# Performance work log

Measured on AMD Instinct MI355X. Metric: run time of the kernel, lower is better.

The kernel has to match this reference:

```python
import jax, jax.numpy as jnp
import numpy as np

SEQ_LEN, BATCH, TAGS = 512, 1024, 32
START_IDX, END_IDX = 30, 31
NEG = -10000.0


def setup_inputs() -> dict:
    key = jax.random.key(0)
    k1, k2 = jax.random.split(key)
    feats = jax.random.normal(k1, (SEQ_LEN, BATCH, TAGS), dtype=jnp.float32)
    mask = jnp.ones((SEQ_LEN, BATCH), dtype=jnp.float32)
    # xavier-normal-ish transition, then apply START/END constraints as in reset_parameters
    transition = jax.random.normal(k2, (TAGS, TAGS), dtype=jnp.float32) * (2.0 / (TAGS + TAGS)) ** 0.5
    transition = transition.at[START_IDX, :].set(NEG)
    transition = transition.at[:, END_IDX].set(NEG)
    return {"feats": feats, "mask": mask, "transition": transition}


def reference(feats, mask, transition):
    # feats: (T, N, M), mask: (T, N), transition: (M, M)
    batch_size, tag_size = feats.shape[1], feats.shape[2]
    alpha0 = jnp.full((batch_size, tag_size), NEG, dtype=feats.dtype)
    alpha0 = alpha0.at[:, START_IDX].set(0.0)

    def step(alpha, inp):
        feat_t, mask_t = inp  # (N, M), (N,)
        # score[n, j, i] = alpha[n, i] + transition[j, i] + feat[n, j]
        score = alpha[:, None, :] + transition[None, :, :] + feat_t[:, :, None]
        new_alpha = jax.nn.logsumexp(score, axis=-1)  # (N, M)
        m = mask_t[:, None]
        alpha = new_alpha * m + alpha * (1.0 - m)
        return alpha, None

    alpha, _ = jax.lax.scan(step, alpha0, (feats, mask))
    alpha = alpha + transition[END_IDX][None, :]
    return jax.nn.logsumexp(alpha, axis=-1)  # (N,)
```

## Files before the change

kernel.cpp:

```cpp
#include <hip/hip_runtime.h>


constexpr int SEQ = 512, BATCH = 1024, TAGS = 32;
constexpr int NC = 8, L = SEQ / NC;
constexpr int RSTRIDE = 36;

#define LOG2E 1.4426950408889634f
#define LN2   0.6931471805599453f

typedef __attribute__((ext_vector_type(8))) short short8;
typedef __attribute__((ext_vector_type(4))) float float4v;
union Frag8 { unsigned u[4]; short8 v; };

__device__ __forceinline__ unsigned pk_rn(float x, float y) {
  return __builtin_amdgcn_perm(__float_as_uint(y) + 0x8000u,
                               __float_as_uint(x) + 0x8000u, 0x07060302u);
}
__device__ __forceinline__ unsigned pk_tr(float x, float y) {
  return __builtin_amdgcn_perm(__float_as_uint(y), __float_as_uint(x), 0x07060302u);
}

__device__ __forceinline__ void mm32(const float* __restrict__ A,
                                     const float* __restrict__ Bs,
                                     int s, int q, float4v D[4]) {
  Frag8 fa0, fa1, fb0, fb1;
  const float* ar0 = A + s * RSTRIDE;
  const float* ar1 = A + (16 + s) * RSTRIDE;
  fa0.u[0] = pk_rn(ar0[4 * q + 0], ar0[4 * q + 1]);
  fa0.u[1] = pk_rn(ar0[4 * q + 2], ar0[4 * q + 3]);
  fa0.u[2] = pk_rn(ar0[16 + 4 * q + 0], ar0[16 + 4 * q + 1]);
  fa0.u[3] = pk_rn(ar0[16 + 4 * q + 2], ar0[16 + 4 * q + 3]);
  fa1.u[0] = pk_rn(ar1[4 * q + 0], ar1[4 * q + 1]);
  fa1.u[1] = pk_rn(ar1[4 * q + 2], ar1[4 * q + 3]);
  fa1.u[2] = pk_rn(ar1[16 + 4 * q + 0], ar1[16 + 4 * q + 1]);
  fa1.u[3] = pk_rn(ar1[16 + 4 * q + 2], ar1[16 + 4 * q + 3]);
  fb0.u[0] = pk_rn(Bs[(4 * q + 0) * RSTRIDE + s], Bs[(4 * q + 1) * RSTRIDE + s]);
  fb0.u[1] = pk_rn(Bs[(4 * q + 2) * RSTRIDE + s], Bs[(4 * q + 3) * RSTRIDE + s]);
  fb0.u[2] = pk_rn(Bs[(16 + 4 * q + 0) * RSTRIDE + s], Bs[(16 + 4 * q + 1) * RSTRIDE + s]);
  fb0.u[3] = pk_rn(Bs[(16 + 4 * q + 2) * RSTRIDE + s], Bs[(16 + 4 * q + 3) * RSTRIDE + s]);
  fb1.u[0] = pk_rn(Bs[(4 * q + 0) * RSTRIDE + 16 + s], Bs[(4 * q + 1) * RSTRIDE + 16 + s]);
  fb1.u[1] = pk_rn(Bs[(4 * q + 2) * RSTRIDE + 16 + s], Bs[(4 * q + 3) * RSTRIDE + 16 + s]);
  fb1.u[2] = pk_rn(Bs[(16 + 4 * q + 0) * RSTRIDE + 16 + s], Bs[(16 + 4 * q + 1) * RSTRIDE + 16 + s]);
  fb1.u[3] = pk_rn(Bs[(16 + 4 * q + 2) * RSTRIDE + 16 + s], Bs[(16 + 4 * q + 3) * RSTRIDE + 16 + s]);
  const float4v z = {0.f, 0.f, 0.f, 0.f};
  D[0] = __builtin_amdgcn_mfma_f32_16x16x32_bf16(fa0.v, fb0.v, z, 0, 0, 0);
  D[1] = __builtin_amdgcn_mfma_f32_16x16x32_bf16(fa0.v, fb1.v, z, 0, 0, 0);
  D[2] = __builtin_amdgcn_mfma_f32_16x16x32_bf16(fa1.v, fb0.v, z, 0, 0, 0);
  D[3] = __builtin_amdgcn_mfma_f32_16x16x32_bf16(fa1.v, fb1.v, z, 0, 0, 0);
}

__device__ __forceinline__ void wrD(float* __restrict__ W, int s, int q,
                                    const float4v D[4]) {
#pragma unroll
  for (int p = 0; p < 4; ++p) {
    W[(4 * q + p) * RSTRIDE + s]           = D[0][p];
    W[(4 * q + p) * RSTRIDE + 16 + s]      = D[1][p];
    W[(16 + 4 * q + p) * RSTRIDE + s]      = D[2][p];
    W[(16 + 4 * q + p) * RSTRIDE + 16 + s] = D[3][p];
  }
}

extern "C" __global__ void __launch_bounds__(512, 4) crf_fused(
    const float* __restrict__ feats, const float* __restrict__ mask,
    const float* __restrict__ trans, float* __restrict__ out) {
  __shared__ float gshare[8][66 * RSTRIDE];
  __shared__ float c2s[8];
  const int wid_u = __builtin_amdgcn_readfirstlane((int)(threadIdx.x >> 6));
  const int lane = threadIdx.x & 63;
  const int b = blockIdx.x;
  const int c = wid_u;
  const int s = lane & 15, q = lane >> 4;
  float* Wf = &gshare[wid_u][0];

  unsigned long long mb;
  {
    const float* fro = feats + ((size_t)(c * L + lane) * BATCH + b) * TAGS;
    float4v fv[8];
#pragma unroll
    for (int i = 0; i < 8; ++i) fv[i] = *(const float4v*)(fro + 4 * i);
    const float mv = mask[(size_t)(c * L + lane) * BATCH + b];
    mb = __ballot(mv != 0.0f);
#pragma unroll
    for (int i = 0; i < 8; ++i) {
      float4v ev;
      ev[0] = __builtin_amdgcn_exp2f(fv[i][0] * LOG2E);
      ev[1] = __builtin_amdgcn_exp2f(fv[i][1] * LOG2E);
      ev[2] = __builtin_amdgcn_exp2f(fv[i][2] * LOG2E);
      ev[3] = __builtin_amdgcn_exp2f(fv[i][3] * LOG2E);
      *(float4v*)(Wf + lane * RSTRIDE + 4 * i) = ev;
    }
  }

  int sig[8];
#pragma unroll
  for (int i = 0; i < 8; ++i) sig[i] = (i < 4) ? (4 * q + i) : (16 + 4 * q + (i - 4));
  Frag8 e0, e1;
#pragma unroll
  for (int p = 0; p < 4; ++p) {
    e0.u[p] = pk_rn(__builtin_amdgcn_exp2f(trans[s * TAGS + sig[2 * p]] * LOG2E),
                    __builtin_amdgcn_exp2f(trans[s * TAGS + sig[2 * p + 1]] * LOG2E));
    e1.u[p] = pk_rn(__builtin_amdgcn_exp2f(trans[(16 + s) * TAGS + sig[2 * p]] * LOG2E),
                    __builtin_amdgcn_exp2f(trans[(16 + s) * TAGS + sig[2 * p + 1]] * LOG2E));
  }
  float ef0[4], ef1[4];
#pragma unroll
  for (int p = 0; p < 4; ++p) {
    ef0[p] = __builtin_amdgcn_exp2f(trans[31 * TAGS + (4 * q + p)] * LOG2E);
    ef1[p] = __builtin_amdgcn_exp2f(trans[31 * TAGS + (16 + 4 * q + p)] * LOG2E);
  }

  float4v P00 = {0,0,0,0}, P01 = {0,0,0,0}, P10 = {0,0,0,0}, P11 = {0,0,0,0};
#pragma unroll
  for (int p = 0; p < 4; ++p) {
    float one = (4 * q + p == s) ? 1.f : 0.f;
    P00[p] = one; P11[p] = one;
  }
  Frag8 B0, B1;
  float c2 = 0.f;
  const float4v zerov = {0.f, 0.f, 0.f, 0.f};

#define PACK_B()                                                        \
  { B0.u[0] = pk_tr(P00[0], P00[1]); B0.u[1] = pk_tr(P00[2], P00[3]);   \
    B0.u[2] = pk_tr(P10[0], P10[1]); B0.u[3] = pk_tr(P10[2], P10[3]);   \
    B1.u[0] = pk_tr(P01[0], P01[1]); B1.u[1] = pk_tr(P01[2], P01[3]);   \
    B1.u[2] = pk_tr(P11[0], P11[1]); B1.u[3] = pk_tr(P11[2], P11[3]); }
  PACK_B()

#define RDF0(t) (*(const float4v*)(Wf + (t) * RSTRIDE + q * 4))
#define RDF1(t) (*(const float4v*)(Wf + (t) * RSTRIDE + 16 + q * 4))

  float4v F0a = RDF0(0), F1a = RDF1(0), F0b = RDF0(1), F1b = RDF1(1);

#pragma unroll 8
  for (int r = 0; r < L; ++r) {
    const float4v F0 = (r & 1) ? F0b : F0a;
    const float4v F1 = (r & 1) ? F1b : F1a;
    if (r & 1) { F0b = RDF0(r + 2); F1b = RDF1(r + 2); }
    else       { F0a = RDF0(r + 2); F1a = RDF1(r + 2); }

    if ((mb >> r) & 1ull) {
      float4v D00 = __builtin_amdgcn_mfma_f32_16x16x32_bf16(e0.v, B0.v, zerov, 0, 0, 0);
      float4v D01 = __builtin_amdgcn_mfma_f32_16x16x32_bf16(e0.v, B1.v, zerov, 0, 0, 0);
      float4v D10 = __builtin_amdgcn_mfma_f32_16x16x32_bf16(e1.v, B0.v, zerov, 0, 0, 0);
      float4v D11 = __builtin_amdgcn_mfma_f32_16x16x32_bf16(e1.v, B1.v, zerov, 0, 0, 0);
      P00 = D00 * F0; P01 = D01 * F0;
      P10 = D10 * F1; P11 = D11 * F1;
      PACK_B()
    }

    if ((r & 7) == 7) {
      float4v m4 = __builtin_elementwise_max(__builtin_elementwise_max(P00, P01),
                                             __builtin_elementwise_max(P10, P11));
      float mx = fmaxf(fmaxf(m4[0], m4[1]), fmaxf(m4[2], m4[3]));
      mx = fmaxf(mx, __shfl_xor(mx, 1, 64));
      mx = fmaxf(mx, __shfl_xor(mx, 2, 64));
      mx = fmaxf(mx, __shfl_xor(mx, 4, 64));
      mx = fmaxf(mx, __shfl_xor(mx, 8, 64));
      mx = fmaxf(mx, __shfl_xor(mx, 16, 64));
      mx = fmaxf(mx, __shfl_xor(mx, 32, 64));
      int ex = (int)((__float_as_uint(mx) >> 23) & 0xFFu) - 127;
      float scl = __uint_as_float((unsigned)(127 - ex) << 23);
      P00 *= scl; P01 *= scl; P10 *= scl; P11 *= scl;
      c2 += (float)ex;
      PACK_B()
    }
  }

  __builtin_amdgcn_s_waitcnt(0);
  __builtin_amdgcn_wave_barrier();
  {
    float4v Pv[4] = {P00, P01, P10, P11};
    wrD(Wf, s, q, Pv);
  }
  if (lane == 0) c2s[wid_u] = c2;
  __syncthreads();

  float4v Dm[4];
  if (wid_u < 4) {
    mm32(&gshare[2 * wid_u + 1][0], &gshare[2 * wid_u][0], s, q, Dm);
    wrD(&gshare[2 * wid_u][0], s, q, Dm);
  }
  __syncthreads();
  if (wid_u < 2) {
    mm32(&gshare[4 * wid_u + 2][0], &gshare[4 * wid_u][0], s, q, Dm);
    wrD(&gshare[4 * wid_u][0], s, q, Dm);
  }
  __syncthreads();
  if (wid_u == 0) {
    mm32(&gshare[4][0], &gshare[0][0], s, q, Dm);
    float vv = 0.f;
#pragma unroll
    for (int p = 0; p < 4; ++p) vv += ef0[p] * Dm[1][p] + ef1[p] * Dm[3][p];
    vv += __shfl_xor(vv, 16, 64);
    vv += __shfl_xor(vv, 32, 64);
    float c2t = ((c2s[0] + c2s[1]) + (c2s[2] + c2s[3])) +
                ((c2s[4] + c2s[5]) + (c2s[6] + c2s[7]));
    if (lane == 14) out[b] = LN2 * (c2t + __builtin_amdgcn_logf(vv));
  }
}

extern "C" void kernel_launch(void* const* d_in, const int* in_sizes, int n_in,
                              void* d_out, int out_size, void* d_ws, size_t ws_size,
                              hipStream_t stream) {
  const float* feats = (const float*)d_in[0];
  const float* mask  = (const float*)d_in[1];
  const float* trans = (const float*)d_in[2];
  float* out = (float*)d_out;
  hipLaunchKernelGGL(crf_fused, dim3(BATCH), dim3(512), 0, stream,
                     feats, mask, trans, out);
}
```

Before: 128.2 us.

## Store exp(feats) as packed bf16 in LDS and replace matrix tree with vector sweep

Exponentiated emissions are now packed in pairs as bf16 into a smaller, XOR-swizzled LDS buffer, which shrinks shared memory per block. That shrinkage lets launch bounds request eight blocks per CU instead of four. The final combine of the eight chunk transfer matrices no longer uses a log-depth tree of 32x32 MFMA products. It instead propagates the END-row vector backwards through each wave's matrix sequentially, with per-step renormalisation. The cost is lower emission precision (bf16 instead of fp32 in the elementwise multiply), eight serialized barrier steps, and possible register pressure from the doubled occupancy target.

```diff
diff --git a/kernel.cpp b/kernel.cpp
--- a/kernel.cpp
+++ b/kernel.cpp
@@ -3,13 +3,14 @@
 
 constexpr int SEQ = 512, BATCH = 1024, TAGS = 32;
 constexpr int NC = 8, L = SEQ / NC;
-constexpr int RSTRIDE = 36;
+constexpr int RROW = 16;
 
 #define LOG2E 1.4426950408889634f
 #define LN2   0.6931471805599453f
 
 typedef __attribute__((ext_vector_type(8))) short short8;
 typedef __attribute__((ext_vector_type(4))) float float4v;
+typedef __attribute__((ext_vector_type(4))) unsigned uint4v;
 union Frag8 { unsigned u[4]; short8 v; };
 
 __device__ __forceinline__ unsigned pk_rn(float x, float y) {
@@ -20,74 +21,43 @@
   return __builtin_amdgcn_perm(__float_as_uint(y), __float_as_uint(x), 0x07060302u);
 }
 
-__device__ __forceinline__ void mm32(const float* __restrict__ A,
-                                     const float* __restrict__ Bs,
-                                     int s, int q, float4v D[4]) {
-  Frag8 fa0, fa1, fb0, fb1;
-  const float* ar0 = A + s * RSTRIDE;
-  const float* ar1 = A + (16 + s) * RSTRIDE;
-  fa0.u[0] = pk_rn(ar0[4 * q + 0], ar0[4 * q + 1]);
-  fa0.u[1] = pk_rn(ar0[4 * q + 2], ar0[4 * q + 3]);
-  fa0.u[2] = pk_rn(ar0[16 + 4 * q + 0], ar0[16 + 4 * q + 1]);
-  fa0.u[3] = pk_rn(ar0[16 + 4 * q + 2], ar0[16 + 4 * q + 3]);
-  fa1.u[0] = pk_rn(ar1[4 * q + 0], ar1[4 * q + 1]);
-  fa1.u[1] = pk_rn(ar1[4 * q + 2], ar1[4 * q + 3]);
-  fa1.u[2] = pk_rn(ar1[16 + 4 * q + 0], ar1[16 + 4 * q + 1]);
-  fa1.u[3] = pk_rn(ar1[16 + 4 * q + 2], ar1[16 + 4 * q + 3]);
-  fb0.u[0] = pk_rn(Bs[(4 * q + 0) * RSTRIDE + s], Bs[(4 * q + 1) * RSTRIDE + s]);
-  fb0.u[1] = pk_rn(Bs[(4 * q + 2) * RSTRIDE + s], Bs[(4 * q + 3) * RSTRIDE + s]);
-  fb0.u[2] = pk_rn(Bs[(16 + 4 * q + 0) * RSTRIDE + s], Bs[(16 + 4 * q + 1) * RSTRIDE + s]);
-  fb0.u[3] = pk_rn(Bs[(16 + 4 * q + 2) * RSTRIDE + s], Bs[(16 + 4 * q + 3) * RSTRIDE + s]);
-  fb1.u[0] = pk_rn(Bs[(4 * q + 0) * RSTRIDE + 16 + s], Bs[(4 * q + 1) * RSTRIDE + 16 + s]);
-  fb1.u[1] = pk_rn(Bs[(4 * q + 2) * RSTRIDE + 16 + s], Bs[(4 * q + 3) * RSTRIDE + 16 + s]);
-  fb1.u[2] = pk_rn(Bs[(16 + 4 * q + 0) * RSTRIDE + 16 + s], Bs[(16 + 4 * q + 1) * RSTRIDE + 16 + s]);
-  fb1.u[3] = pk_rn(Bs[(16 + 4 * q + 2) * RSTRIDE + 16 + s], Bs[(16 + 4 * q + 3) * RSTRIDE + 16 + s]);
-  const float4v z = {0.f, 0.f, 0.f, 0.f};
-  D[0] = __builtin_amdgcn_mfma_f32_16x16x32_bf16(fa0.v, fb0.v, z, 0, 0, 0);
-  D[1] = __builtin_amdgcn_mfma_f32_16x16x32_bf16(fa0.v, fb1.v, z, 0, 0, 0);
-  D[2] = __builtin_amdgcn_mfma_f32_16x16x32_bf16(fa1.v, fb0.v, z, 0, 0, 0);
-  D[3] = __builtin_amdgcn_mfma_f32_16x16x32_bf16(fa1.v, fb1.v, z, 0, 0, 0);
-}
-
-__device__ __forceinline__ void wrD(float* __restrict__ W, int s, int q,
-                                    const float4v D[4]) {
-#pragma unroll
-  for (int p = 0; p < 4; ++p) {
-    W[(4 * q + p) * RSTRIDE + s]           = D[0][p];
-    W[(4 * q + p) * RSTRIDE + 16 + s]      = D[1][p];
-    W[(16 + 4 * q + p) * RSTRIDE + s]      = D[2][p];
-    W[(16 + 4 * q + p) * RSTRIDE + 16 + s] = D[3][p];
-  }
-}
-
-extern "C" __global__ void __launch_bounds__(512, 4) crf_fused(
+extern "C" __global__ void __launch_bounds__(512, 8) crf_fused(
     const float* __restrict__ feats, const float* __restrict__ mask,
     const float* __restrict__ trans, float* __restrict__ out) {
-  __shared__ float gshare[8][66 * RSTRIDE];
-  __shared__ float c2s[8];
-  const int wid_u = __builtin_amdgcn_readfirstlane((int)(threadIdx.x >> 6));
+  __shared__ unsigned gst[NC][66 * RROW];
+  __shared__ float c2s[NC];
+  __shared__ __align__(16) float ws[TAGS];
+  __shared__ float c2x;
+
+  const int wid = __builtin_amdgcn_readfirstlane((int)(threadIdx.x >> 6));
   const int lane = threadIdx.x & 63;
   const int b = blockIdx.x;
-  const int c = wid_u;
   const int s = lane & 15, q = lane >> 4;
-  float* Wf = &gshare[wid_u][0];
+  unsigned* Wp = &gst[wid][0];
 
   unsigned long long mb;
   {
-    const float* fro = feats + ((size_t)(c * L + lane) * BATCH + b) * TAGS;
+    const float* fro = feats + ((size_t)(wid * L + lane) * BATCH + b) * TAGS;
     float4v fv[8];
 #pragma unroll
     for (int i = 0; i < 8; ++i) fv[i] = *(const float4v*)(fro + 4 * i);
-    const float mv = mask[(size_t)(c * L + lane) * BATCH + b];
+    const float mv = mask[(size_t)(wid * L + lane) * BATCH + b];
     mb = __ballot(mv != 0.0f);
+    unsigned Upk[16];
 #pragma unroll
-    for (int i = 0; i < 8; ++i) {
-      float4v ev;
-      ev[0] = __builtin_amdgcn_exp2f(fv[i][0] * LOG2E);
-      ev[1] = __builtin_amdgcn_exp2f(fv[i][1] * LOG2E);
-      ev[2] = __builtin_amdgcn_exp2f(fv[i][2] * LOG2E);
-      ev[3] = __builtin_amdgcn_exp2f(fv[i][3] * LOG2E);
-      *(float4v*)(Wf + lane * RSTRIDE + 4 * i) = ev;
+    for (int j = 0; j < 16; ++j) {
+      const float lo = __builtin_amdgcn_exp2f(fv[j >> 2][j & 3] * LOG2E);
+      const float hi = __builtin_amdgcn_exp2f(fv[4 + (j >> 2)][j & 3] * LOG2E);
+      Upk[j] = pk_rn(lo, hi);
+    }
+    const int swr = ((lane >> 1) & 3) << 2;
+    unsigned* rp = Wp + lane * RROW;
+#pragma unroll
+    for (int g = 0; g < 16; g += 4) {
+      uint4v t;
+#pragma unroll
+      for (int k2 = 0; k2 < 4; ++k2) t[k2] = Upk[(g ^ swr) + k2];
+      *(uint4v*)(rp + g) = t;
     }
   }
 
@@ -102,14 +72,8 @@
     e1.u[p] = pk_rn(__builtin_amdgcn_exp2f(trans[(16 + s) * TAGS + sig[2 * p]] * LOG2E),
                     __builtin_amdgcn_exp2f(trans[(16 + s) * TAGS + sig[2 * p + 1]] * LOG2E));
   }
-  float ef0[4], ef1[4];
-#pragma unroll
-  for (int p = 0; p < 4; ++p) {
-    ef0[p] = __builtin_amdgcn_exp2f(trans[31 * TAGS + (4 * q + p)] * LOG2E);
-    ef1[p] = __builtin_amdgcn_exp2f(trans[31 * TAGS + (16 + 4 * q + p)] * LOG2E);
-  }
 
-  float4v P00 = {0,0,0,0}, P01 = {0,0,0,0}, P10 = {0,0,0,0}, P11 = {0,0,0,0};
+  float4v P00 = {0, 0, 0, 0}, P01 = {0, 0, 0, 0}, P10 = {0, 0, 0, 0}, P11 = {0, 0, 0, 0};
 #pragma unroll
   for (int p = 0; p < 4; ++p) {
     float one = (4 * q + p == s) ? 1.f : 0.f;
@@ -126,19 +90,22 @@
     B1.u[2] = pk_tr(P11[0], P11[1]); B1.u[3] = pk_tr(P11[2], P11[3]); }
   PACK_B()
 
-#define RDF0(t) (*(const float4v*)(Wf + (t) * RSTRIDE + q * 4))
-#define RDF1(t) (*(const float4v*)(Wf + (t) * RSTRIDE + 16 + q * 4))
+#define RDU(t) (*(const uint4v*)(Wp + (t) * RROW + ((4 * q) ^ ((((t) >> 1) & 3) << 2))))
 
-  float4v F0a = RDF0(0), F1a = RDF1(0), F0b = RDF0(1), F1b = RDF1(1);
+  uint4v Ua = RDU(0), Ub = RDU(1);
 
 #pragma unroll 8
   for (int r = 0; r < L; ++r) {
-    const float4v F0 = (r & 1) ? F0b : F0a;
-    const float4v F1 = (r & 1) ? F1b : F1a;
-    if (r & 1) { F0b = RDF0(r + 2); F1b = RDF1(r + 2); }
-    else       { F0a = RDF0(r + 2); F1a = RDF1(r + 2); }
+    const uint4v U = (r & 1) ? Ub : Ua;
+    if (r & 1) Ub = RDU(r + 2); else Ua = RDU(r + 2);
 
     if ((mb >> r) & 1ull) {
+      float4v F0, F1;
+#pragma unroll
+      for (int i = 0; i < 4; ++i) {
+        F0[i] = __uint_as_float(U[i] << 16);
+        F1[i] = __uint_as_float(U[i] & 0xffff0000u);
+      }
       float4v D00 = __builtin_amdgcn_mfma_f32_16x16x32_bf16(e0.v, B0.v, zerov, 0, 0, 0);
       float4v D01 = __builtin_amdgcn_mfma_f32_16x16x32_bf16(e0.v, B1.v, zerov, 0, 0, 0);
       float4v D10 = __builtin_amdgcn_mfma_f32_16x16x32_bf16(e1.v, B0.v, zerov, 0, 0, 0);
@@ -166,36 +133,49 @@
     }
   }
 
-  __builtin_amdgcn_s_waitcnt(0);
-  __builtin_amdgcn_wave_barrier();
-  {
-    float4v Pv[4] = {P00, P01, P10, P11};
-    wrD(Wf, s, q, Pv);
-  }
-  if (lane == 0) c2s[wid_u] = c2;
+  if (lane == 0) c2s[wid] = c2;
+  if (threadIdx.x == 0) c2x = 0.f;
   __syncthreads();
 
-  float4v Dm[4];
-  if (wid_u < 4) {
-    mm32(&gshare[2 * wid_u + 1][0], &gshare[2 * wid_u][0], s, q, Dm);
-    wrD(&gshare[2 * wid_u][0], s, q, Dm);
-  }
-  __syncthreads();
-  if (wid_u < 2) {
-    mm32(&gshare[4 * wid_u + 2][0], &gshare[4 * wid_u][0], s, q, Dm);
-    wrD(&gshare[4 * wid_u][0], s, q, Dm);
-  }
-  __syncthreads();
-  if (wid_u == 0) {
-    mm32(&gshare[4][0], &gshare[0][0], s, q, Dm);
-    float vv = 0.f;
+  for (int k = NC - 1; k >= 0; --k) {
+    if (wid == k) {
+      float4v w0, w1;
+      if (k == NC - 1) {
 #pragma unroll
-    for (int p = 0; p < 4; ++p) vv += ef0[p] * Dm[1][p] + ef1[p] * Dm[3][p];
-    vv += __shfl_xor(vv, 16, 64);
-    vv += __shfl_xor(vv, 32, 64);
-    float c2t = ((c2s[0] + c2s[1]) + (c2s[2] + c2s[3])) +
-                ((c2s[4] + c2s[5]) + (c2s[6] + c2s[7]));
-    if (lane == 14) out[b] = LN2 * (c2t + __builtin_amdgcn_logf(vv));
+        for (int p = 0; p < 4; ++p) {
+          w0[p] = __builtin_amdgcn_exp2f(trans[31 * TAGS + 4 * q + p] * LOG2E);
+          w1[p] = __builtin_amdgcn_exp2f(trans[31 * TAGS + 16 + 4 * q + p] * LOG2E);
+        }
+      } else {
+        w0 = *(const float4v*)(ws + 4 * q);
+        w1 = *(const float4v*)(ws + 16 + 4 * q);
+      }
+      float ps = 0.f, pt = 0.f;
+#pragma unroll
+      for (int p = 0; p < 4; ++p) {
+        ps += w0[p] * P00[p] + w1[p] * P10[p];
+        pt += w0[p] * P01[p] + w1[p] * P11[p];
+      }
+      ps += __shfl_xor(ps, 16, 64); ps += __shfl_xor(ps, 32, 64);
+      pt += __shfl_xor(pt, 16, 64); pt += __shfl_xor(pt, 32, 64);
+      if (k > 0) {
+        float mx = fmaxf(ps, pt);
+        mx = fmaxf(mx, __shfl_xor(mx, 1, 64));
+        mx = fmaxf(mx, __shfl_xor(mx, 2, 64));
+        mx = fmaxf(mx, __shfl_xor(mx, 4, 64));
+        mx = fmaxf(mx, __shfl_xor(mx, 8, 64));
+        int ex = (int)((__float_as_uint(mx) >> 23) & 0xFFu) - 127;
+        float scl = __uint_as_float((unsigned)(127 - ex) << 23);
+        ps *= scl; pt *= scl;
+        if (lane == 0) c2x += (float)ex;
+        if (lane < 16) { ws[lane] = ps; ws[16 + lane] = pt; }
+      } else if (lane == 14) {
+        float c2t = ((c2s[0] + c2s[1]) + (c2s[2] + c2s[3])) +
+                    ((c2s[4] + c2s[5]) + (c2s[6] + c2s[7])) + c2x;
+        out[b] = LN2 * (c2t + __builtin_amdgcn_logf(pt));
+      }
+    }
+    __syncthreads();
   }
 }
 
```

Measured after the change: 139.8 us. 1.09x slower.
